# Optimization experiments

Measured on AMD Instinct MI355X. Metric: run time of the kernel, lower is better.

Reference implementation:

```python
import jax, jax.numpy as jnp
import numpy as np

NUM_GROUPS = 32
EPS = 1e-5


def setup_inputs() -> dict:
    key = jax.random.key(0)
    ks = jax.random.split(key, 4)
    B, C, H, W = 4, 256, 64, 64
    x = jax.random.normal(ks[0], (B, C, H, W), dtype=jnp.float32)
    norm_w = jnp.ones((C,), dtype=jnp.float32)
    norm_b = jnp.zeros((C,), dtype=jnp.float32)
    qkv_w = jax.random.normal(ks[1], (3 * C, C), dtype=jnp.float32) * (C ** -0.5)
    qkv_b = jnp.zeros((3 * C,), dtype=jnp.float32)
    proj_w = jax.random.normal(ks[2], (C, C), dtype=jnp.float32) * (C ** -0.5)
    proj_b = jnp.zeros((C,), dtype=jnp.float32)
    return {"x": x, "norm_w": norm_w, "norm_b": norm_b, "qkv_w": qkv_w,
            "qkv_b": qkv_b, "proj_w": proj_w, "proj_b": proj_b, "num_heads": 1}


def _group_norm(x, w, b):
    B, C, H, W = x.shape
    xg = x.reshape(B, NUM_GROUPS, C // NUM_GROUPS, H, W)
    mean = xg.mean(axis=(2, 3, 4), keepdims=True)
    var = xg.var(axis=(2, 3, 4), keepdims=True)
    xn = ((xg - mean) * jax.lax.rsqrt(var + EPS)).reshape(B, C, H, W)
    return xn * w[None, :, None, None] + b[None, :, None, None]


def reference(x, norm_w, norm_b, qkv_w, qkv_b, proj_w, proj_b, num_heads):
    B, C, H, W = x.shape
    N = H * W
    d = C // num_heads
    xn = _group_norm(x, norm_w, norm_b)
    # 1x1 conv == channel matmul: [B,3C,H,W]
    qkv = jnp.einsum('oc,bchw->bohw', qkv_w, xn) + qkv_b[None, :, None, None]
    qkv = qkv.reshape(B, 3, num_heads, d, N)
    q, k, v = qkv[:, 0], qkv[:, 1], qkv[:, 2]  # each [B,h,d,N]
    scale = d ** -0.5
    attn = jnp.einsum('bhdi,bhdj->bhij', q, k) * scale  # [B,h,N,N]
    attn = jax.nn.softmax(attn, axis=-1)
    out = jnp.einsum('bhij,bhdj->bhdi', attn, v)  # [B,h,d,N]
    out = out.reshape(B, C, H, W)
    out = jnp.einsum('oc,bchw->bohw', proj_w, out) + proj_b[None, :, None, None]
    return x + out
```

## Files before the change

### kernel.cpp

```cpp
#include <hip/hip_runtime.h>
#include <stdint.h>
#include <stddef.h>

#define NB 4
#define NC 256
#define NSP 4096
#define NG 32
#define CPG 8
#define GEPS 1e-5f
#define SCALE 0.0625f
#define NROWS (NB * NSP)
#define JSPLIT 4

typedef __attribute__((ext_vector_type(8))) short s8v;
typedef __attribute__((ext_vector_type(4))) float f4v;
typedef __attribute__((ext_vector_type(16))) float f16v;
typedef __attribute__((ext_vector_type(4))) unsigned short us4v;
typedef __attribute__((ext_vector_type(4))) unsigned int u4v;

__device__ __forceinline__ float b2f(unsigned short h) {
  union { unsigned u; float f; } x; x.u = ((unsigned)h) << 16; return x.f;
}
__device__ __forceinline__ unsigned short f2b(float f) {
  union { float f; unsigned u; } x; x.f = f;
  unsigned r = x.u + 0x7fffu + ((x.u >> 16) & 1u);
  return (unsigned short)(r >> 16);
}
__device__ __forceinline__ unsigned packbf(float lo, float hi) {
  union { float f; unsigned u; } a, b; a.f = lo; b.f = hi;
  return (b.u & 0xffff0000u) | (a.u >> 16);
}

__global__ __launch_bounds__(256) void cvt2_kernel(
    const float* __restrict__ qw, const float* __restrict__ pw,
    unsigned short* __restrict__ wq, unsigned short* __restrict__ wp) {
  int i = (blockIdx.x * 256 + threadIdx.x) * 4;
  const float* src; unsigned short* dst; int j;
  if (i < 3 * NC * NC) { src = qw; dst = wq; j = i; }
  else { src = pw; dst = wp; j = i - 3 * NC * NC; }
  float4 v = *(const float4*)(src + j);
  us4v p;
  p[0] = f2b(v.x); p[1] = f2b(v.y); p[2] = f2b(v.z); p[3] = f2b(v.w);
  *(us4v*)(dst + j) = p;
}

__global__ __launch_bounds__(256) void gn_kernel(
    const float* __restrict__ x, const float* __restrict__ w,
    const float* __restrict__ bias, unsigned short* __restrict__ xn) {
  int b = blockIdx.x >> 5;
  int g = blockIdx.x & 31;
  const float* xp = x + ((size_t)b * NC + (size_t)g * CPG) * NSP;
  int t = threadIdx.x;
  float s = 0.f, ss = 0.f;
  for (int i = 4 * t; i < CPG * NSP; i += 1024) {
    float4 v = *(const float4*)(xp + i);
    s += v.x + v.y + v.z + v.w;
    ss += v.x * v.x + v.y * v.y + v.z * v.z + v.w * v.w;
  }
  __shared__ float r1[256], r2[256];
  r1[t] = s; r2[t] = ss;
  __syncthreads();
  for (int off = 128; off > 0; off >>= 1) {
    if (t < off) { r1[t] += r1[t + off]; r2[t] += r2[t + off]; }
    __syncthreads();
  }
  float mean = r1[0] * (1.f / (CPG * NSP));
  float var  = r2[0] * (1.f / (CPG * NSP)) - mean * mean;
  float rstd = rsqrtf(var + GEPS);
  float wv[CPG], bv[CPG];
  for (int c = 0; c < CPG; c++) {
    wv[c] = w[g * CPG + c] * rstd;
    bv[c] = bias[g * CPG + c] - mean * wv[c];
  }
  for (int n = t; n < NSP; n += 256) {
    s8v pk;
    for (int c = 0; c < CPG; c++) {
      float v = xp[(size_t)c * NSP + n];
      ((unsigned short*)&pk)[c] = f2b(v * wv[c] + bv[c]);
    }
    *(s8v*)(xn + ((size_t)(b * NSP + n) * NC + g * CPG)) = pk;
  }
}

__global__ __launch_bounds__(256) void qkv_gemm(
    const unsigned short* __restrict__ W, const unsigned short* __restrict__ xnG,
    const float* __restrict__ qkvb,
    unsigned short* __restrict__ q, unsigned short* __restrict__ k,
    unsigned short* __restrict__ v) {
  const int sec = blockIdx.y >> 1;
  const int m0 = (blockIdx.y & 1) * 128;
  const int n0 = blockIdx.x * 128;
  const unsigned short* A  = W + (size_t)sec * NC * NC;
  const unsigned short* Bt = xnG + (size_t)blockIdx.z * NSP * NC;
  unsigned short* dst = (sec == 0 ? q : (sec == 1 ? k : v)) + (size_t)blockIdx.z * NSP * NC;
  const float scl = (sec == 0) ? SCALE : 1.f;

  __shared__ unsigned short As[128 * 32], Bs[128 * 32];
  const int t = threadIdx.x;
  const int lane = t & 63, wave = t >> 6;
  const int wm = (wave >> 1) * 64, wn = (wave & 1) * 64;
  const int l16 = lane & 15, quad = lane >> 4;
  const int srow = t >> 2, skc = (t & 3) * 8;

  f4v acc[4][4];
  for (int mi = 0; mi < 4; mi++)
    for (int ni = 0; ni < 4; ni++)
      acc[mi][ni] = (f4v){0.f, 0.f, 0.f, 0.f};

  const unsigned short* Ag0 = A  + (size_t)(m0 + srow) * NC + skc;
  const unsigned short* Ag1 = A  + (size_t)(m0 + srow + 64) * NC + skc;
  const unsigned short* Bg0 = Bt + (size_t)(n0 + srow) * NC + skc;
  const unsigned short* Bg1 = Bt + (size_t)(n0 + srow + 64) * NC + skc;

  for (int k0 = 0; k0 < NC; k0 += 32) {
    s8v a0 = *(const s8v*)(Ag0 + k0);
    s8v a1 = *(const s8v*)(Ag1 + k0);
    s8v b0 = *(const s8v*)(Bg0 + k0);
    s8v b1 = *(const s8v*)(Bg1 + k0);
    __syncthreads();
    *(s8v*)(As + srow * 32 + skc) = a0;
    *(s8v*)(As + (srow + 64) * 32 + skc) = a1;
    *(s8v*)(Bs + srow * 32 + skc) = b0;
    *(s8v*)(Bs + (srow + 64) * 32 + skc) = b1;
    __syncthreads();
    s8v af[4], bfr[4];
    for (int mi = 0; mi < 4; mi++)
      af[mi] = *(const s8v*)(As + (wm + mi * 16 + l16) * 32 + quad * 8);
    for (int ni = 0; ni < 4; ni++)
      bfr[ni] = *(const s8v*)(Bs + (wn + ni * 16 + l16) * 32 + quad * 8);
    for (int mi = 0; mi < 4; mi++)
      for (int ni = 0; ni < 4; ni++)
        acc[mi][ni] = __builtin_amdgcn_mfma_f32_16x16x32_bf16(af[mi], bfr[ni], acc[mi][ni], 0, 0, 0);
  }

  for (int mi = 0; mi < 4; mi++) {
    const int rb = m0 + wm + mi * 16 + quad * 4;
    for (int ni = 0; ni < 4; ni++) {
      const int col = n0 + wn + ni * 16 + l16;
      f4v a = acc[mi][ni];
      if (sec < 2) {
        us4v pk;
        for (int r = 0; r < 4; r++)
          pk[r] = f2b((a[r] + qkvb[sec * NC + rb + r]) * scl);
        const size_t off = (size_t)(col >> 5) * 8192 + (rb >> 4) * 512 +
                           ((rb >> 3) & 1) * 256 + (col & 31) * 8 + (rb & 7);
        *(us4v*)(dst + off) = pk;
      } else {
        for (int r = 0; r < 4; r++) {
          const int d = rb + r;
          const size_t off = (size_t)(col >> 5) * 8192 + (d >> 5) * 1024 +
                             ((col >> 4) & 1) * 512 + ((col >> 3) & 1) * 256 +
                             (d & 31) * 8 + (col & 7);
          dst[off] = f2b(a[r] + qkvb[2 * NC + d]);
        }
      }
    }
  }
}

__global__ __launch_bounds__(256, 2) void flash6_kernel(
    const unsigned short* __restrict__ q, const unsigned short* __restrict__ k,
    const unsigned short* __restrict__ v, unsigned short* __restrict__ Opart,
    float* __restrict__ Lpart) {
  const int qt = blockIdx.x, b = blockIdx.y, js = blockIdx.z;
  const size_t sNC = (size_t)NSP * NC;
  const unsigned short* qb = q + b * sNC;
  const unsigned short* kb = k + b * sNC;
  const unsigned short* vb = v + b * sNC;
  const int t = threadIdx.x, lane = t & 63, w = t >> 6;

  __shared__ unsigned short K_lds[2][16 * 512];
  __shared__ unsigned short V_lds[2][16 * 512];

  f16v zero16;
  #pragma unroll
  for (int r = 0; r < 16; r++) zero16[r] = 0.f;

  s8v qf[16];
  {
    const unsigned short* qp = qb + ((size_t)(qt * 4 + w) * 16) * 512 + lane * 8;
    #pragma unroll
    for (int kc = 0; kc < 16; kc++)
      qf[kc] = *(const s8v*)(qp + kc * 512);
  }

  f16v accO[8];
  #pragma unroll
  for (int dt = 0; dt < 8; dt++) accO[dt] = zero16;
  float l4[4] = {0.f, 0.f, 0.f, 0.f};

  const int jbeg = js * (NSP / JSPLIT);
  const int NT = (NSP / JSPLIT) / 32;

  auto stage = [&](int j0, int bufsel) {
    const size_t tb = (size_t)(j0 >> 5) * 16;
    #pragma unroll
    for (int ii = 0; ii < 8; ii++) {
      const int idx = w * 8 + ii;
      const unsigned short* gp;
      unsigned short* ld;
      if (idx < 16) {
        gp = kb + (tb + idx) * 512 + lane * 8;
        ld = &K_lds[bufsel][idx * 512];
      } else {
        gp = vb + (tb + (idx - 16)) * 512 + lane * 8;
        ld = &V_lds[bufsel][(idx - 16) * 512];
      }
      __builtin_amdgcn_global_load_lds(
          (const __attribute__((address_space(1))) unsigned int*)gp,
          (__attribute__((address_space(3))) unsigned int*)ld, 16, 0, 0);
    }
  };

  stage(jbeg, 0);
  for (int jt = 0; jt < NT; jt++) {
    __syncthreads();
    if (jt + 1 < NT) stage(jbeg + (jt + 1) * 32, (jt + 1) & 1);
    const unsigned short* Kc = K_lds[jt & 1];
    const unsigned short* Vc = V_lds[jt & 1];

    f16v accS = zero16;
    #pragma unroll
    for (int kc = 0; kc < 16; kc++) {
      s8v kf = *(const s8v*)(Kc + kc * 512 + lane * 8);
      accS = __builtin_amdgcn_mfma_f32_32x32x16_bf16(kf, qf[kc], accS, 0, 0, 0);
    }

    float p[16];
    #pragma unroll
    for (int r = 0; r < 16; r++) {
      p[r] = __expf(accS[r]);
      l4[r & 3] += p[r];
    }

    u4v pw0, pw1;
    {
      unsigned a0 = packbf(p[0], p[1]),  b0 = packbf(p[4], p[5]);
      asm("v_permlane32_swap_b32 %0, %1" : "+v"(a0), "+v"(b0));
      unsigned a1 = packbf(p[2], p[3]),  b1 = packbf(p[6], p[7]);
      asm("v_permlane32_swap_b32 %0, %1" : "+v"(a1), "+v"(b1));
      unsigned a2 = packbf(p[8], p[9]),  b2 = packbf(p[12], p[13]);
      asm("v_permlane32_swap_b32 %0, %1" : "+v"(a2), "+v"(b2));
      unsigned a3 = packbf(p[10], p[11]), b3 = packbf(p[14], p[15]);
      asm("v_permlane32_swap_b32 %0, %1" : "+v"(a3), "+v"(b3));
      pw0[0] = a0; pw0[1] = a1; pw0[2] = b0; pw0[3] = b1;
      pw1[0] = a2; pw1[1] = a3; pw1[2] = b2; pw1[3] = b3;
    }
    const s8v pb0 = __builtin_bit_cast(s8v, pw0);
    const s8v pb1 = __builtin_bit_cast(s8v, pw1);

    #pragma unroll
    for (int dt = 0; dt < 8; dt++) {
      s8v vf0 = *(const s8v*)(Vc + dt * 1024 + lane * 8);
      s8v vf1 = *(const s8v*)(Vc + dt * 1024 + 512 + lane * 8);
      accO[dt] = __builtin_amdgcn_mfma_f32_32x32x16_bf16(vf0, pb0, accO[dt], 0, 0, 0);
      accO[dt] = __builtin_amdgcn_mfma_f32_32x32x16_bf16(vf1, pb1, accO[dt], 0, 0, 0);
    }
  }

  float l_acc = l4[0] + l4[1] + l4[2] + l4[3];
  const float ltot = l_acc + __shfl_xor(l_acc, 32, 64);
  const int qrow = b * NSP + qt * 128 + w * 32 + (lane & 31);
  if (lane < 32)
    Lpart[(size_t)js * NROWS + qrow] = ltot;

  unsigned short* Op = Opart + ((size_t)js * NROWS + qrow) * NC;
  const int hi = lane >> 5;
  #pragma unroll
  for (int dt = 0; dt < 8; dt++) {
    #pragma unroll
    for (int g = 0; g < 4; g++) {
      us4v pk;
      #pragma unroll
      for (int r = 0; r < 4; r++)
        pk[r] = f2b(accO[dt][g * 4 + r]);
      *(us4v*)(Op + dt * 32 + g * 8 + hi * 4) = pk;
    }
  }
}

__global__ __launch_bounds__(256) void proj_gemm(
    const unsigned short* __restrict__ Wp, const unsigned short* __restrict__ Opart,
    const float* __restrict__ Lpart, const float* __restrict__ pb,
    const float* __restrict__ x, float* __restrict__ out) {
  const int z = blockIdx.z, m0 = blockIdx.y * 128, n0 = blockIdx.x * 128;
  __shared__ unsigned short As[128 * 32], Bs[128 * 32];
  const int t = threadIdx.x;
  const int lane = t & 63, wave = t >> 6;
  const int wm = (wave >> 1) * 64, wn = (wave & 1) * 64;
  const int l16 = lane & 15, quad = lane >> 4;
  const int srow = t >> 2, skc = (t & 3) * 8;

  const int prow0 = z * NSP + n0 + srow;
  const int prow1 = prow0 + 64;
  float ls0 = 0.f, ls1 = 0.f;
  for (int js = 0; js < JSPLIT; js++) {
    ls0 += Lpart[(size_t)js * NROWS + prow0];
    ls1 += Lpart[(size_t)js * NROWS + prow1];
  }
  const float inv0 = 1.f / ls0, inv1 = 1.f / ls1;

  f4v acc[4][4];
  for (int mi = 0; mi < 4; mi++)
    for (int ni = 0; ni < 4; ni++)
      acc[mi][ni] = (f4v){0.f, 0.f, 0.f, 0.f};

  const unsigned short* Ag0 = Wp + (size_t)(m0 + srow) * NC + skc;
  const unsigned short* Ag1 = Wp + (size_t)(m0 + srow + 64) * NC + skc;

  for (int k0 = 0; k0 < NC; k0 += 32) {
    s8v a0 = *(const s8v*)(Ag0 + k0);
    s8v a1 = *(const s8v*)(Ag1 + k0);
    float bv0[8], bv1[8];
    for (int e = 0; e < 8; e++) { bv0[e] = 0.f; bv1[e] = 0.f; }
    for (int js = 0; js < JSPLIT; js++) {
      const s8v o0 = *(const s8v*)(Opart + ((size_t)js * NROWS + prow0) * NC + k0 + skc);
      const s8v o1 = *(const s8v*)(Opart + ((size_t)js * NROWS + prow1) * NC + k0 + skc);
      for (int e = 0; e < 8; e++) {
        bv0[e] += b2f(((const unsigned short*)&o0)[e]);
        bv1[e] += b2f(((const unsigned short*)&o1)[e]);
      }
    }
    s8v b0, b1;
    for (int e = 0; e < 8; e++) {
      ((unsigned short*)&b0)[e] = f2b(bv0[e] * inv0);
      ((unsigned short*)&b1)[e] = f2b(bv1[e] * inv1);
    }
    __syncthreads();
    *(s8v*)(As + srow * 32 + skc) = a0;
    *(s8v*)(As + (srow + 64) * 32 + skc) = a1;
    *(s8v*)(Bs + srow * 32 + skc) = b0;
    *(s8v*)(Bs + (srow + 64) * 32 + skc) = b1;
    __syncthreads();
    s8v af[4], bfr[4];
    for (int mi = 0; mi < 4; mi++)
      af[mi] = *(const s8v*)(As + (wm + mi * 16 + l16) * 32 + quad * 8);
    for (int ni = 0; ni < 4; ni++)
      bfr[ni] = *(const s8v*)(Bs + (wn + ni * 16 + l16) * 32 + quad * 8);
    for (int mi = 0; mi < 4; mi++)
      for (int ni = 0; ni < 4; ni++)
        acc[mi][ni] = __builtin_amdgcn_mfma_f32_16x16x32_bf16(af[mi], bfr[ni], acc[mi][ni], 0, 0, 0);
  }

  float* C = out + (size_t)z * NC * NSP;
  const float* R = x + (size_t)z * NC * NSP;
  for (int mi = 0; mi < 4; mi++) {
    const int rb = m0 + wm + mi * 16 + quad * 4;
    for (int ni = 0; ni < 4; ni++) {
      const int col = n0 + wn + ni * 16 + l16;
      f4v a = acc[mi][ni];
      for (int r = 0; r < 4; r++)
        C[(size_t)(rb + r) * NSP + col] =
            a[r] + pb[rb + r] + R[(size_t)(rb + r) * NSP + col];
    }
  }
}

extern "C" void kernel_launch(void* const* d_in, const int* in_sizes, int n_in,
                              void* d_out, int out_size, void* d_ws, size_t ws_size,
                              hipStream_t stream) {
  const float* x      = (const float*)d_in[0];
  const float* norm_w = (const float*)d_in[1];
  const float* norm_b = (const float*)d_in[2];
  const float* qkv_w  = (const float*)d_in[3];
  const float* qkv_b  = (const float*)d_in[4];
  const float* proj_w = (const float*)d_in[5];
  const float* proj_b = (const float*)d_in[6];
  float* out = (float*)d_out;

  char* ws = (char*)d_ws;
  unsigned short* wq = (unsigned short*)ws;
  unsigned short* wp = (unsigned short*)(ws + 3 * NC * NC * 2);
  char* wst = ws + (1 << 20);
  const size_t szBNC = (size_t)NB * NSP * NC * 2;
  unsigned short* xn = (unsigned short*)wst;
  unsigned short* q  = (unsigned short*)(wst + szBNC);
  unsigned short* k  = (unsigned short*)(wst + 2 * szBNC);
  unsigned short* v  = (unsigned short*)(wst + 3 * szBNC);
  unsigned short* Opart = (unsigned short*)(wst + 4 * szBNC);
  float* Lpart = (float*)(wst + 4 * szBNC + (size_t)JSPLIT * NROWS * NC * 2);

  cvt2_kernel<<<dim3(4 * NC * NC / 1024), 256, 0, stream>>>(qkv_w, proj_w, wq, wp);
  gn_kernel<<<dim3(NB * NG), 256, 0, stream>>>(x, norm_w, norm_b, xn);
  qkv_gemm<<<dim3(NSP / 128, 6, NB), 256, 0, stream>>>(wq, xn, qkv_b, q, k, v);
  flash6_kernel<<<dim3(NSP / 128, NB, JSPLIT), 256, 0, stream>>>(q, k, v, Opart, Lpart);
  proj_gemm<<<dim3(NSP / 128, NC / 128, NB), 256, 0, stream>>>(
      wp, Opart, Lpart, proj_b, x, out);
}
```

Before: 209.3 us.

## Process two query tiles per wave in flash attention to reuse K/V fragments

Each wave now holds two 32-row query tiles and computes both against every K/V fragment it reads from LDS, so each block covers 256 query rows instead of 128 and launches half as many blocks. This halves LDS reads and K/V global staging per query row and gives the scheduler two independent MFMA chains to interleave. The cost is roughly double the register footprint (two sets of Q fragments and output accumulators), so launch bounds drop to one block per SIMD set, which lowers occupancy. With fewer blocks (256 total) the load may also balance less evenly across CUs.

```diff
diff --git a/kernel.cpp b/kernel.cpp
--- a/kernel.cpp
+++ b/kernel.cpp
@@ -158,7 +158,7 @@
   }
 }
 
-__global__ __launch_bounds__(256, 2) void flash6_kernel(
+__global__ __launch_bounds__(256, 1) void flash7_kernel(
     const unsigned short* __restrict__ q, const unsigned short* __restrict__ k,
     const unsigned short* __restrict__ v, unsigned short* __restrict__ Opart,
     float* __restrict__ Lpart) {
@@ -176,18 +176,20 @@
   #pragma unroll
   for (int r = 0; r < 16; r++) zero16[r] = 0.f;
 
-  s8v qf[16];
+  s8v qfA[16], qfB[16];
   {
-    const unsigned short* qp = qb + ((size_t)(qt * 4 + w) * 16) * 512 + lane * 8;
-    #pragma unroll
-    for (int kc = 0; kc < 16; kc++)
-      qf[kc] = *(const s8v*)(qp + kc * 512);
-  }
-
-  f16v accO[8];
+    const unsigned short* qpA = qb + (size_t)(qt * 8 + w * 2) * 8192 + lane * 8;
+    #pragma unroll
+    for (int kc = 0; kc < 16; kc++) {
+      qfA[kc] = *(const s8v*)(qpA + kc * 512);
+      qfB[kc] = *(const s8v*)(qpA + 8192 + kc * 512);
+    }
+  }
+
+  f16v accOA[8], accOB[8];
   #pragma unroll
-  for (int dt = 0; dt < 8; dt++) accO[dt] = zero16;
-  float l4[4] = {0.f, 0.f, 0.f, 0.f};
+  for (int dt = 0; dt < 8; dt++) { accOA[dt] = zero16; accOB[dt] = zero16; }
+  float lA[4] = {0.f, 0.f, 0.f, 0.f}, lB[4] = {0.f, 0.f, 0.f, 0.f};
 
   const int jbeg = js * (NSP / JSPLIT);
   const int NT = (NSP / JSPLIT) / 32;
@@ -219,63 +221,95 @@
     const unsigned short* Kc = K_lds[jt & 1];
     const unsigned short* Vc = V_lds[jt & 1];
 
-    f16v accS = zero16;
+    f16v sA = zero16, sB = zero16;
     #pragma unroll
     for (int kc = 0; kc < 16; kc++) {
       s8v kf = *(const s8v*)(Kc + kc * 512 + lane * 8);
-      accS = __builtin_amdgcn_mfma_f32_32x32x16_bf16(kf, qf[kc], accS, 0, 0, 0);
-    }
-
-    float p[16];
+      sA = __builtin_amdgcn_mfma_f32_32x32x16_bf16(kf, qfA[kc], sA, 0, 0, 0);
+      sB = __builtin_amdgcn_mfma_f32_32x32x16_bf16(kf, qfB[kc], sB, 0, 0, 0);
+    }
+
     #pragma unroll
     for (int r = 0; r < 16; r++) {
-      p[r] = __expf(accS[r]);
-      l4[r & 3] += p[r];
-    }
-
-    u4v pw0, pw1;
+      sA[r] = __expf(sA[r]); lA[r & 3] += sA[r];
+      sB[r] = __expf(sB[r]); lB[r & 3] += sB[r];
+    }
+
+    s8v pbA0, pbA1, pbB0, pbB1;
     {
-      unsigned a0 = packbf(p[0], p[1]),  b0 = packbf(p[4], p[5]);
+      u4v w0, w1;
+      unsigned a0 = packbf(sA[0], sA[1]),   b0 = packbf(sA[4], sA[5]);
       asm("v_permlane32_swap_b32 %0, %1" : "+v"(a0), "+v"(b0));
-      unsigned a1 = packbf(p[2], p[3]),  b1 = packbf(p[6], p[7]);
+      unsigned a1 = packbf(sA[2], sA[3]),   b1 = packbf(sA[6], sA[7]);
       asm("v_permlane32_swap_b32 %0, %1" : "+v"(a1), "+v"(b1));
-      unsigned a2 = packbf(p[8], p[9]),  b2 = packbf(p[12], p[13]);
+      unsigned a2 = packbf(sA[8], sA[9]),   b2 = packbf(sA[12], sA[13]);
       asm("v_permlane32_swap_b32 %0, %1" : "+v"(a2), "+v"(b2));
-      unsigned a3 = packbf(p[10], p[11]), b3 = packbf(p[14], p[15]);
+      unsigned a3 = packbf(sA[10], sA[11]), b3 = packbf(sA[14], sA[15]);
       asm("v_permlane32_swap_b32 %0, %1" : "+v"(a3), "+v"(b3));
-      pw0[0] = a0; pw0[1] = a1; pw0[2] = b0; pw0[3] = b1;
-      pw1[0] = a2; pw1[1] = a3; pw1[2] = b2; pw1[3] = b3;
-    }
-    const s8v pb0 = __builtin_bit_cast(s8v, pw0);
-    const s8v pb1 = __builtin_bit_cast(s8v, pw1);
+      w0[0] = a0; w0[1] = a1; w0[2] = b0; w0[3] = b1;
+      w1[0] = a2; w1[1] = a3; w1[2] = b2; w1[3] = b3;
+      pbA0 = __builtin_bit_cast(s8v, w0);
+      pbA1 = __builtin_bit_cast(s8v, w1);
+    }
+    {
+      u4v w0, w1;
+      unsigned a0 = packbf(sB[0], sB[1]),   b0 = packbf(sB[4], sB[5]);
+      asm("v_permlane32_swap_b32 %0, %1" : "+v"(a0), "+v"(b0));
+      unsigned a1 = packbf(sB[2], sB[3]),   b1 = packbf(sB[6], sB[7]);
+      asm("v_permlane32_swap_b32 %0, %1" : "+v"(a1), "+v"(b1));
+      unsigned a2 = packbf(sB[8], sB[9]),   b2 = packbf(sB[12], sB[13]);
+      asm("v_permlane32_swap_b32 %0, %1" : "+v"(a2), "+v"(b2));
+      unsigned a3 = packbf(sB[10], sB[11]), b3 = packbf(sB[14], sB[15]);
+      asm("v_permlane32_swap_b32 %0, %1" : "+v"(a3), "+v"(b3));
+      w0[0] = a0; w0[1] = a1; w0[2] = b0; w0[3] = b1;
+      w1[0] = a2; w1[1] = a3; w1[2] = b2; w1[3] = b3;
+      pbB0 = __builtin_bit_cast(s8v, w0);
+      pbB1 = __builtin_bit_cast(s8v, w1);
+    }
 
     #pragma unroll
     for (int dt = 0; dt < 8; dt++) {
       s8v vf0 = *(const s8v*)(Vc + dt * 1024 + lane * 8);
       s8v vf1 = *(const s8v*)(Vc + dt * 1024 + 512 + lane * 8);
-      accO[dt] = __builtin_amdgcn_mfma_f32_32x32x16_bf16(vf0, pb0, accO[dt], 0, 0, 0);
-      accO[dt] = __builtin_amdgcn_mfma_f32_32x32x16_bf16(vf1, pb1, accO[dt], 0, 0, 0);
-    }
-  }
-
-  float l_acc = l4[0] + l4[1] + l4[2] + l4[3];
-  const float ltot = l_acc + __shfl_xor(l_acc, 32, 64);
-  const int qrow = b * NSP + qt * 128 + w * 32 + (lane & 31);
-  if (lane < 32)
-    Lpart[(size_t)js * NROWS + qrow] = ltot;
-
-  unsigned short* Op = Opart + ((size_t)js * NROWS + qrow) * NC;
+      accOA[dt] = __builtin_amdgcn_mfma_f32_32x32x16_bf16(vf0, pbA0, accOA[dt], 0, 0, 0);
+      accOB[dt] = __builtin_amdgcn_mfma_f32_32x32x16_bf16(vf0, pbB0, accOB[dt], 0, 0, 0);
+      accOA[dt] = __builtin_amdgcn_mfma_f32_32x32x16_bf16(vf1, pbA1, accOA[dt], 0, 0, 0);
+      accOB[dt] = __builtin_amdgcn_mfma_f32_32x32x16_bf16(vf1, pbB1, accOB[dt], 0, 0, 0);
+    }
+  }
+
   const int hi = lane >> 5;
-  #pragma unroll
-  for (int dt = 0; dt < 8; dt++) {
-    #pragma unroll
-    for (int g = 0; g < 4; g++) {
-      us4v pk;
+  {
+    float la = lA[0] + lA[1] + lA[2] + lA[3];
+    const float ltot = la + __shfl_xor(la, 32, 64);
+    const int qrow = b * NSP + qt * 256 + w * 64 + (lane & 31);
+    if (lane < 32) Lpart[(size_t)js * NROWS + qrow] = ltot;
+    unsigned short* Op = Opart + ((size_t)js * NROWS + qrow) * NC;
+    #pragma unroll
+    for (int dt = 0; dt < 8; dt++)
       #pragma unroll
-      for (int r = 0; r < 4; r++)
-        pk[r] = f2b(accO[dt][g * 4 + r]);
-      *(us4v*)(Op + dt * 32 + g * 8 + hi * 4) = pk;
-    }
+      for (int g = 0; g < 4; g++) {
+        us4v pk;
+        #pragma unroll
+        for (int r = 0; r < 4; r++) pk[r] = f2b(accOA[dt][g * 4 + r]);
+        *(us4v*)(Op + dt * 32 + g * 8 + hi * 4) = pk;
+      }
+  }
+  {
+    float lb = lB[0] + lB[1] + lB[2] + lB[3];
+    const float ltot = lb + __shfl_xor(lb, 32, 64);
+    const int qrow = b * NSP + qt * 256 + w * 64 + 32 + (lane & 31);
+    if (lane < 32) Lpart[(size_t)js * NROWS + qrow] = ltot;
+    unsigned short* Op = Opart + ((size_t)js * NROWS + qrow) * NC;
+    #pragma unroll
+    for (int dt = 0; dt < 8; dt++)
+      #pragma unroll
+      for (int g = 0; g < 4; g++) {
+        us4v pk;
+        #pragma unroll
+        for (int r = 0; r < 4; r++) pk[r] = f2b(accOB[dt][g * 4 + r]);
+        *(us4v*)(Op + dt * 32 + g * 8 + hi * 4) = pk;
+      }
   }
 }
 
@@ -383,7 +417,7 @@
   cvt2_kernel<<<dim3(4 * NC * NC / 1024), 256, 0, stream>>>(qkv_w, proj_w, wq, wp);
   gn_kernel<<<dim3(NB * NG), 256, 0, stream>>>(x, norm_w, norm_b, xn);
   qkv_gemm<<<dim3(NSP / 128, 6, NB), 256, 0, stream>>>(wq, xn, qkv_b, q, k, v);
-  flash6_kernel<<<dim3(NSP / 128, NB, JSPLIT), 256, 0, stream>>>(q, k, v, Opart, Lpart);
+  flash7_kernel<<<dim3(NSP / 256, NB, JSPLIT), 256, 0, stream>>>(q, k, v, Opart, Lpart);
   proj_gemm<<<dim3(NSP / 128, NC / 128, NB), 256, 0, stream>>>(
       wp, Opart, Lpart, proj_b, x, out);
 }
```

Measured after the change: 213.3 us. Within noise of the previous version (+1.9%).

## Load K and V fragments directly from global memory, dropping LDS staging

Applied to the files above, without the earlier changes.

The attention kernel no longer stages K/V tiles into double-buffered LDS with async global-to-LDS loads and barriers. Each wave instead reads its MFMA K and V fragments straight from global memory, where the data is already in fragment-friendly order. This removes the __syncthreads and the LDS traffic and frees LDS. The cost is that the four waves each fetch the same K/V tiles, so reuse depends on L1/L2, and the loads are no longer prefetched one tile ahead, which exposes global latency.

```diff
diff --git a/kernel.cpp b/kernel.cpp
--- a/kernel.cpp
+++ b/kernel.cpp
@@ -158,7 +158,7 @@
   }
 }
 
-__global__ __launch_bounds__(256, 2) void flash6_kernel(
+__global__ __launch_bounds__(256, 2) void flash9_kernel(
     const unsigned short* __restrict__ q, const unsigned short* __restrict__ k,
     const unsigned short* __restrict__ v, unsigned short* __restrict__ Opart,
     float* __restrict__ Lpart) {
@@ -169,16 +169,13 @@
   const unsigned short* vb = v + b * sNC;
   const int t = threadIdx.x, lane = t & 63, w = t >> 6;
 
-  __shared__ unsigned short K_lds[2][16 * 512];
-  __shared__ unsigned short V_lds[2][16 * 512];
-
   f16v zero16;
   #pragma unroll
   for (int r = 0; r < 16; r++) zero16[r] = 0.f;
 
   s8v qf[16];
   {
-    const unsigned short* qp = qb + ((size_t)(qt * 4 + w) * 16) * 512 + lane * 8;
+    const unsigned short* qp = qb + (size_t)(qt * 4 + w) * 8192 + lane * 8;
     #pragma unroll
     for (int kc = 0; kc < 16; kc++)
       qf[kc] = *(const s8v*)(qp + kc * 512);
@@ -189,40 +186,17 @@
   for (int dt = 0; dt < 8; dt++) accO[dt] = zero16;
   float l4[4] = {0.f, 0.f, 0.f, 0.f};
 
-  const int jbeg = js * (NSP / JSPLIT);
-  const int NT = (NSP / JSPLIT) / 32;
-
-  auto stage = [&](int j0, int bufsel) {
-    const size_t tb = (size_t)(j0 >> 5) * 16;
-    #pragma unroll
-    for (int ii = 0; ii < 8; ii++) {
-      const int idx = w * 8 + ii;
-      const unsigned short* gp;
-      unsigned short* ld;
-      if (idx < 16) {
-        gp = kb + (tb + idx) * 512 + lane * 8;
-        ld = &K_lds[bufsel][idx * 512];
-      } else {
-        gp = vb + (tb + (idx - 16)) * 512 + lane * 8;
-        ld = &V_lds[bufsel][(idx - 16) * 512];
-      }
-      __builtin_amdgcn_global_load_lds(
-          (const __attribute__((address_space(1))) unsigned int*)gp,
-          (__attribute__((address_space(3))) unsigned int*)ld, 16, 0, 0);
-    }
-  };
-
-  stage(jbeg, 0);
-  for (int jt = 0; jt < NT; jt++) {
-    __syncthreads();
-    if (jt + 1 < NT) stage(jbeg + (jt + 1) * 32, (jt + 1) & 1);
-    const unsigned short* Kc = K_lds[jt & 1];
-    const unsigned short* Vc = V_lds[jt & 1];
+  const int tbeg = (js * (NSP / JSPLIT)) >> 5;
+  const int tcnt = (NSP / JSPLIT) >> 5;
+
+  for (int tt = tbeg; tt < tbeg + tcnt; tt++) {
+    const unsigned short* Kt = kb + (size_t)tt * 8192 + lane * 8;
+    const unsigned short* Vt = vb + (size_t)tt * 8192 + lane * 8;
 
     f16v accS = zero16;
     #pragma unroll
     for (int kc = 0; kc < 16; kc++) {
-      s8v kf = *(const s8v*)(Kc + kc * 512 + lane * 8);
+      s8v kf = *(const s8v*)(Kt + kc * 512);
       accS = __builtin_amdgcn_mfma_f32_32x32x16_bf16(kf, qf[kc], accS, 0, 0, 0);
     }
 
@@ -235,11 +209,11 @@
 
     u4v pw0, pw1;
     {
-      unsigned a0 = packbf(p[0], p[1]),  b0 = packbf(p[4], p[5]);
+      unsigned a0 = packbf(p[0], p[1]),   b0 = packbf(p[4], p[5]);
       asm("v_permlane32_swap_b32 %0, %1" : "+v"(a0), "+v"(b0));
-      unsigned a1 = packbf(p[2], p[3]),  b1 = packbf(p[6], p[7]);
+      unsigned a1 = packbf(p[2], p[3]),   b1 = packbf(p[6], p[7]);
       asm("v_permlane32_swap_b32 %0, %1" : "+v"(a1), "+v"(b1));
-      unsigned a2 = packbf(p[8], p[9]),  b2 = packbf(p[12], p[13]);
+      unsigned a2 = packbf(p[8], p[9]),   b2 = packbf(p[12], p[13]);
       asm("v_permlane32_swap_b32 %0, %1" : "+v"(a2), "+v"(b2));
       unsigned a3 = packbf(p[10], p[11]), b3 = packbf(p[14], p[15]);
       asm("v_permlane32_swap_b32 %0, %1" : "+v"(a3), "+v"(b3));
@@ -251,8 +225,8 @@
 
     #pragma unroll
     for (int dt = 0; dt < 8; dt++) {
-      s8v vf0 = *(const s8v*)(Vc + dt * 1024 + lane * 8);
-      s8v vf1 = *(const s8v*)(Vc + dt * 1024 + 512 + lane * 8);
+      s8v vf0 = *(const s8v*)(Vt + dt * 1024);
+      s8v vf1 = *(const s8v*)(Vt + dt * 1024 + 512);
       accO[dt] = __builtin_amdgcn_mfma_f32_32x32x16_bf16(vf0, pb0, accO[dt], 0, 0, 0);
       accO[dt] = __builtin_amdgcn_mfma_f32_32x32x16_bf16(vf1, pb1, accO[dt], 0, 0, 0);
     }
@@ -383,7 +357,7 @@
   cvt2_kernel<<<dim3(4 * NC * NC / 1024), 256, 0, stream>>>(qkv_w, proj_w, wq, wp);
   gn_kernel<<<dim3(NB * NG), 256, 0, stream>>>(x, norm_w, norm_b, xn);
   qkv_gemm<<<dim3(NSP / 128, 6, NB), 256, 0, stream>>>(wq, xn, qkv_b, q, k, v);
-  flash6_kernel<<<dim3(NSP / 128, NB, JSPLIT), 256, 0, stream>>>(q, k, v, Opart, Lpart);
+  flash9_kernel<<<dim3(NSP / 128, NB, JSPLIT), 256, 0, stream>>>(q, k, v, Opart, Lpart);
   proj_gemm<<<dim3(NSP / 128, NC / 128, NB), 256, 0, stream>>>(
       wp, Opart, Lpart, proj_b, x, out);
 }
```

New measurement: 302.4 us. 1.44x slower.
